# Kernel tuning notes

Measured on AMD Instinct MI355X. Metric: run time of the kernel, lower is better.

Reference implementation:

```python
import jax, jax.numpy as jnp
import numpy as np

B, H, S, DK = 2, 16, 2048, 64


def setup_inputs() -> dict:
    key = jax.random.key(0)
    kq, kk, kv = jax.random.split(key, 3)
    query = jax.random.normal(kq, (B, H, S, DK), dtype=jnp.float32)
    k = jax.random.normal(kk, (B, H, S, DK), dtype=jnp.float32)
    value = jax.random.normal(kv, (B, H, S, DK), dtype=jnp.float32)
    # causal padding-style mask: 1 = keep, 0 = masked (set to -inf pre-softmax)
    mask = jnp.tril(jnp.ones((S, S), dtype=jnp.int32))[None, None, :, :]
    return {"query": query, "key": k, "value": value, "d_k": DK, "mask": mask}


def reference(query, key, value, d_k, mask):
    # scores: [B, H, Sq, Sk]
    scores = jnp.einsum("bhqd,bhkd->bhqk", query, key)
    scores = scores / jnp.sqrt(jnp.asarray(d_k, dtype=scores.dtype))
    scores = jnp.where(mask == 0, -jnp.inf, scores)
    att = jax.nn.softmax(scores, axis=-1)
    # dropout is identity in eval mode (deterministic reference)
    out = jnp.einsum("bhqk,bhkd->bhqd", att, value)
    return out
```

## Files before the change

kernel.cpp:

```cpp
#include <hip/hip_runtime.h>
#include <cstdint>

#define B_ 2
#define H_ 16
#define S_ 2048
#define DK_ 64
#define BH_ (B_*H_)
#define NQT 32

typedef __attribute__((ext_vector_type(8))) short short8;
typedef __attribute__((ext_vector_type(4))) short short4v;
typedef __attribute__((ext_vector_type(4))) float floatx4;

__device__ inline unsigned short f2bf(float f) {
  union { float f; unsigned u; } v; v.f = f;
  unsigned u = v.u;
  unsigned r = u + 0x7fffu + ((u >> 16) & 1u);
  return (unsigned short)(r >> 16);
}

__device__ inline floatx4 mfma16(short4v a, short4v b, floatx4 c) {
#if __has_builtin(__builtin_amdgcn_mfma_f32_16x16x16bf16_1k)
  return __builtin_amdgcn_mfma_f32_16x16x16bf16_1k(a, b, c, 0, 0, 0);
#else
  asm("v_mfma_f32_16x16x16_bf16 %0, %1, %2, %0" : "+v"(c) : "v"(a), "v"(b));
  return c;
#endif
}

__device__ inline short4v u2s4(unsigned a, unsigned b) {
  union { unsigned u[2]; short4v s; } v;
  v.u[0] = a; v.u[1] = b;
  return v.s;
}

__global__ __launch_bounds__(256) void conv_kv(const float* __restrict__ K,
                                               const float* __restrict__ V,
                                               unsigned short* __restrict__ Kb,
                                               unsigned short* __restrict__ Vb) {
  __shared__ __align__(16) unsigned short t[64 * 80];
  const int bh = blockIdx.y, s0 = blockIdx.x * 64;
  const int row = threadIdx.x >> 2, cp = threadIdx.x & 3;

  {
    const float* src = K + ((size_t)(bh * S_ + s0 + row)) * DK_ + cp * 16;
    unsigned short* dst = Kb + ((size_t)(bh * S_ + s0 + row)) * DK_ + cp * 16;
    #pragma unroll
    for (int h = 0; h < 2; ++h) {
      float4 a = *(const float4*)(src + h * 8);
      float4 b = *(const float4*)(src + h * 8 + 4);
      uint4 st;
      st.x = (unsigned)f2bf(a.x) | ((unsigned)f2bf(a.y) << 16);
      st.y = (unsigned)f2bf(a.z) | ((unsigned)f2bf(a.w) << 16);
      st.z = (unsigned)f2bf(b.x) | ((unsigned)f2bf(b.y) << 16);
      st.w = (unsigned)f2bf(b.z) | ((unsigned)f2bf(b.w) << 16);
      *(uint4*)(dst + h * 8) = st;
    }
  }
  {
    const float* src = V + ((size_t)(bh * S_ + s0 + row)) * DK_ + cp * 16;
    #pragma unroll
    for (int j4 = 0; j4 < 4; ++j4) {
      float4 a = *(const float4*)(src + j4 * 4);
      int c = cp * 16 + j4 * 4;
      t[(c + 0) * 80 + row] = f2bf(a.x);
      t[(c + 1) * 80 + row] = f2bf(a.y);
      t[(c + 2) * 80 + row] = f2bf(a.z);
      t[(c + 3) * 80 + row] = f2bf(a.w);
    }
    __syncthreads();
    unsigned short* dst = Vb + ((size_t)(bh * DK_ + row)) * S_ + s0 + cp * 16;
    *(uint4*)(dst + 0) = *(const uint4*)&t[row * 80 + cp * 16];
    *(uint4*)(dst + 8) = *(const uint4*)&t[row * 80 + cp * 16 + 8];
  }
}

__global__ __launch_bounds__(256, 3)
void fa_kernel(const float* __restrict__ Q, const unsigned short* __restrict__ Kb,
               const unsigned short* __restrict__ Vb, float* __restrict__ Out) {
  __shared__ floatx4 OredV[4 * 2 * 4 * 64];
  __shared__ float   Lred[4 * 4 * 16];

  const int tid  = threadIdx.x;
  const int wave = tid >> 6;
  const int lane = tid & 63;
  const int quad = lane >> 4;
  const int l16  = lane & 15;

  const int id = blockIdx.x;
  const int bh = (id & 7) | (((id >> 3) & 3) << 3);
  const int qt = NQT - 1 - (id >> 5);
  const int nkv = qt + 1;

  const float SCL = 0.125f * 1.44269504088896340736f;

  short8 qf[8];
  #pragma unroll
  for (int nq = 0; nq < 4; ++nq) {
    const float* p = Q + ((size_t)bh * S_ + qt * 64 + nq * 16 + l16) * DK_ + quad * 8;
    #pragma unroll
    for (int ks = 0; ks < 2; ++ks) {
      float4 x = *(const float4*)(p + ks * 32);
      float4 y = *(const float4*)(p + ks * 32 + 4);
      short8 t;
      t[0]=(short)f2bf(x.x*SCL); t[1]=(short)f2bf(x.y*SCL); t[2]=(short)f2bf(x.z*SCL); t[3]=(short)f2bf(x.w*SCL);
      t[4]=(short)f2bf(y.x*SCL); t[5]=(short)f2bf(y.y*SCL); t[6]=(short)f2bf(y.z*SCL); t[7]=(short)f2bf(y.w*SCL);
      qf[nq * 2 + ks] = t;
    }
  }

  floatx4 Ot[4][4];
  float ls[4] = {0.f, 0.f, 0.f, 0.f};
  #pragma unroll
  for (int d = 0; d < 4; ++d)
    #pragma unroll
    for (int nq = 0; nq < 4; ++nq) Ot[d][nq] = (floatx4){0,0,0,0};

  const unsigned short* pK = Kb + (((size_t)bh * S_ + wave * 16 + l16) << 6) + quad * 8;
  const unsigned short* pV = Vb + (((size_t)bh * DK_ + l16) << 11) + wave * 16 + quad * 4;

  short8  ck0 = *(const short8*)pK;
  short8  ck1 = *(const short8*)(pK + 32);
  short4v cv0 = *(const short4v*)(pV);
  short4v cv1 = *(const short4v*)(pV + 16 * 2048);
  short4v cv2 = *(const short4v*)(pV + 32 * 2048);
  short4v cv3 = *(const short4v*)(pV + 48 * 2048);

  for (int kv = 0; kv < nkv; ++kv) {
    const bool last = (kv == nkv - 1);
    short8 nk0, nk1; short4v nv0, nv1, nv2, nv3;
    if (!last) {
      pK += 4096; pV += 64;
      nk0 = *(const short8*)pK;
      nk1 = *(const short8*)(pK + 32);
      nv0 = *(const short4v*)(pV);
      nv1 = *(const short4v*)(pV + 16 * 2048);
      nv2 = *(const short4v*)(pV + 32 * 2048);
      nv3 = *(const short4v*)(pV + 48 * 2048);
    }
    unsigned pk[4][2];
    #pragma unroll
    for (int nq = 0; nq < 4; ++nq) {
      if (last && nq < wave) continue;
      floatx4 s0 = (floatx4){0,0,0,0};
      __builtin_amdgcn_s_setprio(1);
      s0 = __builtin_amdgcn_mfma_f32_16x16x32_bf16(ck0, qf[nq * 2 + 0], s0, 0, 0, 0);
      s0 = __builtin_amdgcn_mfma_f32_16x16x32_bf16(ck1, qf[nq * 2 + 1], s0, 0, 0, 0);
      __builtin_amdgcn_s_setprio(0);
      if (last && nq == wave) {
        #pragma unroll
        for (int r = 0; r < 4; ++r)
          if (quad * 4 + r > l16) s0[r] = -INFINITY;
      }
      float e0 = __builtin_amdgcn_exp2f(s0[0]);
      float e1 = __builtin_amdgcn_exp2f(s0[1]);
      float e2 = __builtin_amdgcn_exp2f(s0[2]);
      float e3 = __builtin_amdgcn_exp2f(s0[3]);
      ls[nq] += (e0 + e1) + (e2 + e3);
      pk[nq][0] = __builtin_amdgcn_perm(__float_as_uint(e1) + 0x8000u,
                                        __float_as_uint(e0) + 0x8000u, 0x07060302u);
      pk[nq][1] = __builtin_amdgcn_perm(__float_as_uint(e3) + 0x8000u,
                                        __float_as_uint(e2) + 0x8000u, 0x07060302u);
    }
    __builtin_amdgcn_s_setprio(1);
    #pragma unroll
    for (int nq = 0; nq < 4; ++nq) {
      if (last && nq < wave) continue;
      const short4v pb = u2s4(pk[nq][0], pk[nq][1]);
      Ot[0][nq] = mfma16(cv0, pb, Ot[0][nq]);
      Ot[1][nq] = mfma16(cv1, pb, Ot[1][nq]);
      Ot[2][nq] = mfma16(cv2, pb, Ot[2][nq]);
      Ot[3][nq] = mfma16(cv3, pb, Ot[3][nq]);
    }
    __builtin_amdgcn_s_setprio(0);
    if (!last) { ck0 = nk0; ck1 = nk1; cv0 = nv0; cv1 = nv1; cv2 = nv2; cv3 = nv3; }
  }

  #pragma unroll
  for (int nq = 0; nq < 4; ++nq) {
    ls[nq] += __shfl_xor(ls[nq], 16);
    ls[nq] += __shfl_xor(ls[nq], 32);
  }
  if (lane < 16) {
    #pragma unroll
    for (int nq = 0; nq < 4; ++nq) Lred[(wave * 4 + nq) * 16 + lane] = ls[nq];
  }
  float inv = 0.f;
  #pragma unroll
  for (int rnd = 0; rnd < 2; ++rnd) {
    #pragma unroll
    for (int db = 0; db < 2; ++db)
      #pragma unroll
      for (int nq = 0; nq < 4; ++nq)
        OredV[((wave * 2 + db) * 4 + nq) * 64 + lane] = Ot[rnd * 2 + db][nq];
    __syncthreads();
    if (rnd == 0) {
      const float lt = Lred[(0 * 4 + wave) * 16 + l16] + Lred[(1 * 4 + wave) * 16 + l16]
                     + Lred[(2 * 4 + wave) * 16 + l16] + Lred[(3 * 4 + wave) * 16 + l16];
      inv = 1.0f / lt;
    }
    #pragma unroll
    for (int db = 0; db < 2; ++db) {
      floatx4 s = OredV[((0 * 2 + db) * 4 + wave) * 64 + lane]
                + OredV[((1 * 2 + db) * 4 + wave) * 64 + lane]
                + OredV[((2 * 2 + db) * 4 + wave) * 64 + lane]
                + OredV[((3 * 2 + db) * 4 + wave) * 64 + lane];
      s *= inv;
      *(floatx4*)(Out + ((size_t)(bh * S_ + qt * 64 + wave * 16 + l16)) * 64
                      + (rnd * 2 + db) * 16 + quad * 4) = s;
    }
    if (rnd == 0) __syncthreads();
  }
}

extern "C" void kernel_launch(void* const* d_in, const int* in_sizes, int n_in,
                              void* d_out, int out_size, void* d_ws, size_t ws_size,
                              hipStream_t stream) {
  const float* Q = (const float*)d_in[0];
  const float* K = (const float*)d_in[1];
  const float* V = (const float*)d_in[2];
  float* Out = (float*)d_out;
  unsigned short* Kb = (unsigned short*)d_ws;
  unsigned short* Vb = Kb + (size_t)BH_ * S_ * DK_;
  conv_kv<<<dim3(S_ / 64, BH_), 256, 0, stream>>>(K, V, Kb, Vb);
  fa_kernel<<<dim3(NQT * BH_), 256, 0, stream>>>(Q, Kb, Vb, Out);
}
```

Baseline: 163.3 us.

## Stage K/V tiles through triple-buffered LDS via async global_load_lds

Replaces the per-wave register prefetch of K and V fragments from global memory with a 3-slot LDS ring buffer. Each KV tile is loaded cooperatively with global_load_lds two iterations ahead, using an XOR swizzle so the LDS reads are conflict-free. The loop synchronises with vmcnt waits and a barrier per iteration. This cuts redundant global traffic, since all waves share one tile copy instead of each loading its own fragment, and hides load latency. The cost is a block-wide barrier every iteration and 48KB of LDS, which may limit occupancy against the target of 3 blocks.

```diff
diff --git a/kernel.cpp b/kernel.cpp
--- a/kernel.cpp
+++ b/kernel.cpp
@@ -78,8 +78,7 @@
 __global__ __launch_bounds__(256, 3)
 void fa_kernel(const float* __restrict__ Q, const unsigned short* __restrict__ Kb,
                const unsigned short* __restrict__ Vb, float* __restrict__ Out) {
-  __shared__ floatx4 OredV[4 * 2 * 4 * 64];
-  __shared__ float   Lred[4 * 4 * 16];
+  __shared__ __align__(16) unsigned short SMEM[6 * 4096];
 
   const int tid  = threadIdx.x;
   const int wave = tid >> 6;
@@ -116,28 +115,40 @@
     #pragma unroll
     for (int nq = 0; nq < 4; ++nq) Ot[d][nq] = (floatx4){0,0,0,0};
 
-  const unsigned short* pK = Kb + (((size_t)bh * S_ + wave * 16 + l16) << 6) + quad * 8;
-  const unsigned short* pV = Vb + (((size_t)bh * DK_ + l16) << 11) + wave * 16 + quad * 4;
-
-  short8  ck0 = *(const short8*)pK;
-  short8  ck1 = *(const short8*)(pK + 32);
-  short4v cv0 = *(const short4v*)(pV);
-  short4v cv1 = *(const short4v*)(pV + 16 * 2048);
-  short4v cv2 = *(const short4v*)(pV + 32 * 2048);
-  short4v cv3 = *(const short4v*)(pV + 48 * 2048);
-
-  for (int kv = 0; kv < nkv; ++kv) {
-    const bool last = (kv == nkv - 1);
-    short8 nk0, nk1; short4v nv0, nv1, nv2, nv3;
-    if (!last) {
-      pK += 4096; pV += 64;
-      nk0 = *(const short8*)pK;
-      nk1 = *(const short8*)(pK + 32);
-      nv0 = *(const short4v*)(pV);
-      nv1 = *(const short4v*)(pV + 16 * 2048);
-      nv2 = *(const short4v*)(pV + 32 * 2048);
-      nv3 = *(const short4v*)(pV + 48 * 2048);
-    }
+  auto stage = [&](int buf, int kv) {
+    unsigned short* Ktb = SMEM + buf * 4096;
+    unsigned short* Vtb = SMEM + (3 + buf) * 4096;
+    #pragma unroll
+    for (int rd = 0; rd < 2; ++rd) {
+      const int cid = rd * 256 + wave * 64 + lane;
+      const int row = cid >> 3;
+      const int c   = (cid & 7) ^ (row & 7);
+      {
+        const unsigned short* g = Kb + (((size_t)bh * S_ + kv * 64 + row) << 6) + (c << 3);
+        __builtin_amdgcn_global_load_lds(
+            (const __attribute__((address_space(1))) void*)g,
+            (__attribute__((address_space(3))) void*)&Ktb[(rd * 4 + wave) * 512], 16, 0, 0);
+      }
+      {
+        const unsigned short* g = Vb + (((size_t)(bh * DK_ + row)) << 11) + kv * 64 + (c << 3);
+        __builtin_amdgcn_global_load_lds(
+            (const __attribute__((address_space(1))) void*)g,
+            (__attribute__((address_space(3))) void*)&Vtb[(rd * 4 + wave) * 512], 16, 0, 0);
+      }
+    }
+  };
+
+  auto computeT = [&](int cur, bool last) {
+    const unsigned short* Ktc = SMEM + cur * 4096;
+    const unsigned short* Vtc = SMEM + (3 + cur) * 4096;
+    const int rk = wave * 16 + l16;
+    const short8 ck0 = *(const short8*)&Ktc[rk * 64 + ((quad    ) ^ (l16 & 7)) * 8];
+    const short8 ck1 = *(const short8*)&Ktc[rk * 64 + ((quad + 4) ^ (l16 & 7)) * 8];
+    short4v cv[4];
+    #pragma unroll
+    for (int dblk = 0; dblk < 4; ++dblk)
+      cv[dblk] = *(const short4v*)&Vtc[(dblk * 16 + l16) * 64 +
+                    ((wave * 2 + (quad >> 1)) ^ (l16 & 7)) * 8 + (quad & 1) * 4];
     unsigned pk[4][2];
     #pragma unroll
     for (int nq = 0; nq < 4; ++nq) {
@@ -167,20 +178,34 @@
     for (int nq = 0; nq < 4; ++nq) {
       if (last && nq < wave) continue;
       const short4v pb = u2s4(pk[nq][0], pk[nq][1]);
-      Ot[0][nq] = mfma16(cv0, pb, Ot[0][nq]);
-      Ot[1][nq] = mfma16(cv1, pb, Ot[1][nq]);
-      Ot[2][nq] = mfma16(cv2, pb, Ot[2][nq]);
-      Ot[3][nq] = mfma16(cv3, pb, Ot[3][nq]);
+      Ot[0][nq] = mfma16(cv[0], pb, Ot[0][nq]);
+      Ot[1][nq] = mfma16(cv[1], pb, Ot[1][nq]);
+      Ot[2][nq] = mfma16(cv[2], pb, Ot[2][nq]);
+      Ot[3][nq] = mfma16(cv[3], pb, Ot[3][nq]);
     }
     __builtin_amdgcn_s_setprio(0);
-    if (!last) { ck0 = nk0; ck1 = nk1; cv0 = nv0; cv1 = nv1; cv2 = nv2; cv3 = nv3; }
-  }
-
+  };
+
+  stage(0, 0);
+  if (nkv > 1) stage(1, 1);
+  int cur = 0;
+  for (int kv = 0; kv < nkv; ++kv) {
+    if (kv + 1 < nkv) asm volatile("s_waitcnt vmcnt(4)" ::: "memory");
+    else              asm volatile("s_waitcnt vmcnt(0)" ::: "memory");
+    __builtin_amdgcn_s_barrier();
+    if (kv + 2 < nkv) stage(cur == 0 ? 2 : cur - 1, kv + 2);
+    computeT(cur, kv == nkv - 1);
+    cur = (cur == 2) ? 0 : cur + 1;
+  }
+
+  floatx4* OredV = (floatx4*)SMEM;
+  float*   Lred  = (float*)SMEM + 8192;
   #pragma unroll
   for (int nq = 0; nq < 4; ++nq) {
     ls[nq] += __shfl_xor(ls[nq], 16);
     ls[nq] += __shfl_xor(ls[nq], 32);
   }
+  __syncthreads();
   if (lane < 16) {
     #pragma unroll
     for (int nq = 0; nq < 4; ++nq) Lred[(wave * 4 + nq) * 16 + lane] = ls[nq];
```

Result: faster. 144.5 us (-11.5%).
